# Kernel tuning notes

Measured on AMD Instinct MI355X. Metric: run time of the kernel, lower is better.

The kernel has to match this reference:

```python
import jax, jax.numpy as jnp
import numpy as np

B, T, HID = 2, 2048, 1536
H, HKV, D = 12, 2, 128
EPS = 1e-6
NEG = -1e9


def setup_inputs() -> dict:
    key = jax.random.key(0)
    ks = jax.random.split(key, 8)
    # rotary embeddings built from real angles (cos/sin of position*inv_freq)
    inv_freq = 1.0 / (10000.0 ** (jnp.arange(0, D, 2, dtype=jnp.float32) / D))  # [D/2]
    pos = jnp.arange(T, dtype=jnp.float32)
    ang = pos[:, None] * inv_freq[None, :]                       # [T, D/2]
    emb = jnp.concatenate([ang, ang], axis=-1)                   # [T, D]
    cos = jnp.broadcast_to(jnp.cos(emb)[None], (B, T, D))
    sin = jnp.broadcast_to(jnp.sin(emb)[None], (B, T, D))
    # additive causal mask [1,1,T,T]
    causal = jnp.tril(jnp.ones((T, T), dtype=bool))
    attention_mask = jnp.where(causal, 0.0, NEG).astype(jnp.float32)[None, None]
    s = 0.02
    return {
        "hidden_states": jax.random.normal(ks[0], (B, T, HID), jnp.float32),
        "cos": cos,
        "sin": sin,
        "attention_mask": attention_mask,
        "q_w": jax.random.normal(ks[1], (H * D, HID), jnp.float32) * s,
        "k_w": jax.random.normal(ks[2], (HKV * D, HID), jnp.float32) * s,
        "v_w": jax.random.normal(ks[3], (HKV * D, HID), jnp.float32) * s,
        "o_w": jax.random.normal(ks[4], (HID, H * D), jnp.float32) * s,
        "q_norm_w": jnp.ones((D,), jnp.float32),
        "k_norm_w": jnp.ones((D,), jnp.float32),
    }


def _rms_norm(x, w):
    # per-head RMSNorm over last dim (head_dim), computed in fp32
    xf = x.astype(jnp.float32)
    var = jnp.mean(xf * xf, axis=-1, keepdims=True)
    return (w * (xf * jax.lax.rsqrt(var + EPS))).astype(x.dtype)


def _rotate_half(x):
    x1, x2 = jnp.split(x, 2, axis=-1)
    return jnp.concatenate([-x2, x1], axis=-1)


def reference(hidden_states, cos, sin, attention_mask, q_w, k_w, v_w, o_w, q_norm_w, k_norm_w):
    b, t, _ = hidden_states.shape
    n_rep = H // HKV
    scale = D ** -0.5

    # projections -> [B, n_heads, T, D]
    q = (hidden_states @ q_w.T).reshape(b, t, H, D)
    k = (hidden_states @ k_w.T).reshape(b, t, HKV, D)
    v = (hidden_states @ v_w.T).reshape(b, t, HKV, D).transpose(0, 2, 1, 3)

    # per-head QK RMSNorm, then to [B, H, T, D]
    q = _rms_norm(q, q_norm_w).transpose(0, 2, 1, 3)
    k = _rms_norm(k, k_norm_w).transpose(0, 2, 1, 3)

    # RoPE (cos/sin broadcast over head axis)
    c = cos[:, None, :, :]
    s = sin[:, None, :, :]
    q = q * c + _rotate_half(q) * s
    k = k * c + _rotate_half(k) * s

    # GQA repeat_kv: [B, HKV, T, D] -> [B, H, T, D]
    k = jnp.repeat(k, n_rep, axis=1)
    v = jnp.repeat(v, n_rep, axis=1)

    attn = jnp.einsum('bhqd,bhkd->bhqk', q, k) * scale + attention_mask
    attn = jax.nn.softmax(attn.astype(jnp.float32), axis=-1).astype(q.dtype)
    out = jnp.einsum('bhqk,bhkd->bhqd', attn, v)
    out = out.transpose(0, 2, 1, 3).reshape(b, t, H * D)
    return out @ o_w.T
```

## Files before the change

### kernel.cpp

```cpp
#include <hip/hip_runtime.h>
#include <hip/hip_bf16.h>


#define B_   2
#define T_   2048
#define HID_ 1536
#define H_   12
#define HKV_ 2
#define D_   128
#define GQ_  (H_ / HKV_)
#define NQKV_ 2048
#define SCALE_ 0.08838834764831845f

typedef unsigned short u16;
typedef __attribute__((ext_vector_type(4))) float f32x4;
typedef __attribute__((ext_vector_type(8))) short bf16x8;
typedef __attribute__((ext_vector_type(4))) unsigned short u16x4;
typedef __attribute__((ext_vector_type(8))) unsigned short u16x8;

__device__ __forceinline__ u16 f2b(float f) {
  union { __hip_bfloat16 h; u16 u; } cv;
  cv.h = __float2bfloat16(f);
  return cv.u;
}
__device__ __forceinline__ float b2f(u16 u) {
  union { float f; unsigned i; } cv;
  cv.i = ((unsigned)u) << 16;
  return cv.f;
}

__device__ __forceinline__ void glds16(const u16* g, u16* l) {
  __builtin_amdgcn_global_load_lds((const __attribute__((address_space(1))) void*)g,
                                   (__attribute__((address_space(3))) void*)l, 16, 0, 0);
}

__global__ __launch_bounds__(256) void cvt_f32_bf16(const float* __restrict__ src,
                                                    u16* __restrict__ dst, int n4) {
  int i = blockIdx.x * 256 + threadIdx.x;
  const int stride = gridDim.x * 256;
  for (; i < n4; i += stride) {
    const float4 v = reinterpret_cast<const float4*>(src)[i];
    u16x4 o = {f2b(v.x), f2b(v.y), f2b(v.z), f2b(v.w)};
    reinterpret_cast<u16x4*>(dst)[i] = o;
  }
}

__device__ __forceinline__ void cstore(float* p, float v) { *p = v; }
__device__ __forceinline__ void cstore(u16* p, float v) { *p = f2b(v); }

template <typename CT>
__global__ __launch_bounds__(256) void gemm_bt(const u16* __restrict__ A,
                                               const u16* __restrict__ W,
                                               CT* __restrict__ C,
                                               int M, int N, int K) {
  __shared__ __align__(16) u16 As[128 * 32];
  __shared__ __align__(16) u16 Ws[128 * 32];
  const int tid  = threadIdx.x;
  const int lane = tid & 63;
  const int wid  = tid >> 6;
  const int wr = wid >> 1, wc = wid & 1;
  const int l15 = lane & 15, kg = lane >> 4;
  const int rowBase = blockIdx.y * 128;
  const int colBase = blockIdx.x * 128;

  const int srow = lane >> 2;
  const int scol = (lane & 3) << 3;
  const u16* Ab = A + (size_t)(rowBase + wid * 16 + srow) * K + scol;
  const u16* Wb = W + (size_t)(colBase + wid * 16 + srow) * K + scol;
  u16* AsW = &As[wid * 512];
  u16* WsW = &Ws[wid * 512];

  const f32x4 zero4 = {0.f, 0.f, 0.f, 0.f};
  f32x4 acc[4][4];
#pragma unroll
  for (int m = 0; m < 4; ++m)
#pragma unroll
    for (int n = 0; n < 4; ++n) acc[m][n] = zero4;

  for (int k0 = 0; k0 < K; k0 += 32) {
    __syncthreads();
    glds16(Ab + k0, AsW);
    glds16(Ab + (size_t)64 * K + k0, AsW + 2048);
    glds16(Wb + k0, WsW);
    glds16(Wb + (size_t)64 * K + k0, WsW + 2048);
    __syncthreads();
    bf16x8 a[4], b[4];
#pragma unroll
    for (int m = 0; m < 4; ++m)
      a[m] = *reinterpret_cast<const bf16x8*>(&As[(wr * 64 + m * 16 + l15) * 32 + kg * 8]);
#pragma unroll
    for (int n = 0; n < 4; ++n)
      b[n] = *reinterpret_cast<const bf16x8*>(&Ws[(wc * 64 + n * 16 + l15) * 32 + kg * 8]);
#pragma unroll
    for (int m = 0; m < 4; ++m)
#pragma unroll
      for (int n = 0; n < 4; ++n)
        acc[m][n] = __builtin_amdgcn_mfma_f32_16x16x32_bf16(a[m], b[n], acc[m][n], 0, 0, 0);
  }
#pragma unroll
  for (int m = 0; m < 4; ++m) {
    const int row0 = rowBase + wr * 64 + m * 16 + kg * 4;
#pragma unroll
    for (int n = 0; n < 4; ++n) {
      const int col = colBase + wc * 64 + n * 16 + l15;
#pragma unroll
      for (int r = 0; r < 4; ++r) cstore(&C[(size_t)(row0 + r) * N + col], acc[m][n][r]);
    }
  }
}

__global__ __launch_bounds__(256) void norm_rope_cvt(
    const u16* __restrict__ qkv, const float* __restrict__ cosb,
    const float* __restrict__ sinb, const float* __restrict__ q_nw,
    const float* __restrict__ k_nw, u16* __restrict__ q_b,
    u16* __restrict__ k_b, u16* __restrict__ vt_b) {
  const int gwave = (int)((blockIdx.x * 256 + threadIdx.x) >> 6);
  const int lane = threadIdx.x & 63;
  const int NQ = B_ * T_ * H_;
  const int NK = B_ * T_ * HKV_;
  if (gwave < NQ) {
    const int bt = gwave / H_, h = gwave - bt * H_;
    const u16* src = qkv + (size_t)bt * NQKV_ + h * D_;
    const float x1 = b2f(src[lane]), x2 = b2f(src[lane + 64]);
    float ss = x1 * x1 + x2 * x2;
#pragma unroll
    for (int m = 32; m >= 1; m >>= 1) ss += __shfl_xor(ss, m);
    const float rinv = rsqrtf(ss * (1.0f / D_) + 1e-6f);
    const float c1 = cosb[(size_t)bt * D_ + lane], c2 = cosb[(size_t)bt * D_ + lane + 64];
    const float s1 = sinb[(size_t)bt * D_ + lane], s2 = sinb[(size_t)bt * D_ + lane + 64];
    const float n1 = x1 * rinv * q_nw[lane], n2 = x2 * rinv * q_nw[lane + 64];
    const float o1 = (n1 * c1 - n2 * s1) * SCALE_;
    const float o2 = (n2 * c2 + n1 * s2) * SCALE_;
    const int b = bt >> 11, t = bt & (T_ - 1);
    u16* dst = q_b + ((size_t)(b * H_ + h) * T_ + t) * D_;
    dst[lane] = f2b(o1);
    dst[lane + 64] = f2b(o2);
  } else if (gwave < NQ + NK) {
    const int r = gwave - NQ;
    const int bt = r >> 1, hv = r & 1;
    const u16* src = qkv + (size_t)bt * NQKV_ + 1536 + hv * D_;
    const float x1 = b2f(src[lane]), x2 = b2f(src[lane + 64]);
    float ss = x1 * x1 + x2 * x2;
#pragma unroll
    for (int m = 32; m >= 1; m >>= 1) ss += __shfl_xor(ss, m);
    const float rinv = rsqrtf(ss * (1.0f / D_) + 1e-6f);
    const float c1 = cosb[(size_t)bt * D_ + lane], c2 = cosb[(size_t)bt * D_ + lane + 64];
    const float s1 = sinb[(size_t)bt * D_ + lane], s2 = sinb[(size_t)bt * D_ + lane + 64];
    const float n1 = x1 * rinv * k_nw[lane], n2 = x2 * rinv * k_nw[lane + 64];
    const float o1 = n1 * c1 - n2 * s1;
    const float o2 = n2 * c2 + n1 * s2;
    const int b = bt >> 11, t = bt & (T_ - 1);
    u16* dst = k_b + ((size_t)(b * HKV_ + hv) * T_ + t) * D_;
    dst[lane] = f2b(o1);
    dst[lane + 64] = f2b(o2);
  } else {
    const int r = gwave - NQ - NK;
    const int bt = r >> 1, hv = r & 1;
    const u16* src = qkv + (size_t)bt * NQKV_ + 1792 + hv * D_;
    const float x1 = b2f(src[lane]), x2 = b2f(src[lane + 64]);
    const int b = bt >> 11, t = bt & (T_ - 1);
    const int kk = t & 63;
    const int tp = (t & ~63) | (kk & 32) | (((kk >> 2) & 3) << 3) |
                   (((kk >> 4) & 1) << 2) | (kk & 3);
    u16* dst = vt_b + (size_t)(b * HKV_ + hv) * D_ * T_;
    dst[(size_t)lane * T_ + tp] = f2b(x1);
    dst[(size_t)(lane + 64) * T_ + tp] = f2b(x2);
  }
}

__global__ __launch_bounds__(256) void attn_kernel(const u16* __restrict__ q_b,
                                                   const u16* __restrict__ k_b,
                                                   const u16* __restrict__ vt_b,
                                                   u16* __restrict__ aout,
                                                   u16* __restrict__ po0,
                                                   float2* __restrict__ ml) {
  __shared__ __align__(16) u16 Ks[2][64 * 128];
  __shared__ __align__(16) u16 Vs[2][128 * 64];
  const int bh = blockIdx.x;
  const int y = blockIdx.y;
  const int qt = (y < 16) ? y : (y - 8);
  const int s = (y < 16) ? 0 : 1;
  const int kt0 = s * 16;
  const int ktend = (s == 0) ? min(2 * qt + 1, 15) : (2 * qt + 1);
  const bool splitq = (qt >= 8);
  const int b = bh / H_, h = bh - b * H_;
  const int kvh = h / GQ_;
  const int tid = threadIdx.x;
  const int w = tid >> 6, lane = tid & 63;
  const int l15 = lane & 15, kg = lane >> 4;
  const int qbase = qt * 128;

  const u16* Kb = k_b + (size_t)(b * HKV_ + kvh) * T_ * D_;
  const u16* Vb = vt_b + (size_t)(b * HKV_ + kvh) * D_ * T_;

  bf16x8 qf[2][4];
#pragma unroll
  for (int qb = 0; qb < 2; ++qb) {
    const u16* qrow =
        q_b + ((size_t)(b * H_ + h) * T_ + qbase + w * 32 + qb * 16 + l15) * D_;
#pragma unroll
    for (int s4 = 0; s4 < 4; ++s4)
      qf[qb][s4] = *reinterpret_cast<const bf16x8*>(qrow + s4 * 32 + kg * 8);
  }

  int kK[4], vK[4];
#pragma unroll
  for (int c = 0; c < 4; ++c) {
    const int ch = w * 4 + c;
    const int kr = ch * 4 + (lane >> 4);
    kK[c] = kr * D_ + (((lane & 15) << 3) ^ ((kr & 7) << 3));
    const int dr = ch * 8 + (lane >> 3);
    vK[c] = dr * T_ + (((lane & 7) << 3) ^ ((dr & 7) << 3));
  }

  const int xorv = (l15 & 7) << 3;

  const f32x4 zero4 = {0.f, 0.f, 0.f, 0.f};
  f32x4 o[2][8];
#pragma unroll
  for (int qb = 0; qb < 2; ++qb)
#pragma unroll
    for (int n = 0; n < 8; ++n) o[qb][n] = zero4;
  float m[2] = {0.f, 0.f};
  float lsum[2] = {0.f, 0.f};

  {
    const size_t kb = (size_t)kt0 * 64;
#pragma unroll
    for (int c = 0; c < 4; ++c) {
      glds16(Kb + kb * D_ + kK[c], &Ks[0][(w * 4 + c) * 512]);
      glds16(Vb + kb + vK[c], &Vs[0][(w * 4 + c) * 512]);
    }
  }
  __syncthreads();
  int cur = 0;

  for (int kt = kt0; kt <= ktend; ++kt) {
    if (kt < ktend) {
      const size_t kb = (size_t)(kt + 1) * 64;
#pragma unroll
      for (int c = 0; c < 4; ++c) {
        glds16(Kb + kb * D_ + kK[c], &Ks[cur ^ 1][(w * 4 + c) * 512]);
        glds16(Vb + kb + vK[c], &Vs[cur ^ 1][(w * 4 + c) * 512]);
      }
    }
    f32x4 sc[2][4];
#pragma unroll
    for (int qb = 0; qb < 2; ++qb)
#pragma unroll
      for (int n = 0; n < 4; ++n) sc[qb][n] = zero4;
#pragma unroll
    for (int n = 0; n < 4; ++n)
#pragma unroll
      for (int s4 = 0; s4 < 4; ++s4) {
        const int koff = (n * 16 + l15) * 128 + ((s4 * 32 + kg * 8) ^ xorv);
        bf16x8 kf = *reinterpret_cast<const bf16x8*>(&Ks[cur][koff]);
#pragma unroll
        for (int qb = 0; qb < 2; ++qb)
          sc[qb][n] = __builtin_amdgcn_mfma_f32_16x16x32_bf16(kf, qf[qb][s4],
                                                              sc[qb][n], 0, 0, 0);
      }
    if (kt >= 2 * qt) {
#pragma unroll
      for (int qb = 0; qb < 2; ++qb) {
        const int qg = w * 32 + qb * 16 + l15;
        const int kbb = (kt - 2 * qt) * 64;
#pragma unroll
        for (int n = 0; n < 4; ++n)
#pragma unroll
          for (int r = 0; r < 4; ++r)
            if (kbb + n * 16 + kg * 4 + r > qg) sc[qb][n][r] = -3e38f;
      }
    }
    float pm[2];
#pragma unroll
    for (int qb = 0; qb < 2; ++qb) {
      float v = sc[qb][0][0];
#pragma unroll
      for (int n = 0; n < 4; ++n)
#pragma unroll
        for (int r = 0; r < 4; ++r) v = fmaxf(v, sc[qb][n][r]);
      v = fmaxf(v, __shfl_xor(v, 16));
      v = fmaxf(v, __shfl_xor(v, 32));
      pm[qb] = v;
    }
    if (__any((pm[0] > m[0] + 8.f) | (pm[1] > m[1] + 8.f))) {
#pragma unroll
      for (int qb = 0; qb < 2; ++qb) {
        const float mn = fmaxf(m[qb], pm[qb]);
        const float al = __expf(m[qb] - mn);
        m[qb] = mn;
        lsum[qb] *= al;
        float alT[4];
#pragma unroll
        for (int r = 0; r < 4; ++r)
          alT[r] = __shfl(al, (lane & 48) | (kg * 4 + r));
#pragma unroll
        for (int n = 0; n < 8; ++n)
#pragma unroll
          for (int r = 0; r < 4; ++r) o[qb][n][r] *= alT[r];
      }
    }
#pragma unroll
    for (int qb = 0; qb < 2; ++qb) {
      float rs = 0.f;
#pragma unroll
      for (int n = 0; n < 4; ++n)
#pragma unroll
        for (int r = 0; r < 4; ++r) {
          const float p = __expf(sc[qb][n][r] - m[qb]);
          sc[qb][n][r] = p;
          rs += p;
        }
      rs += __shfl_xor(rs, 16);
      rs += __shfl_xor(rs, 32);
      lsum[qb] += rs;
    }
    bf16x8 pf[2][2];
#pragma unroll
    for (int qb = 0; qb < 2; ++qb)
#pragma unroll
      for (int ks = 0; ks < 2; ++ks)
#pragma unroll
        for (int r = 0; r < 4; ++r) {
          pf[qb][ks][r] = (short)f2b(sc[qb][2 * ks][r]);
          pf[qb][ks][r + 4] = (short)f2b(sc[qb][2 * ks + 1][r]);
        }
#pragma unroll
    for (int n = 0; n < 8; ++n)
#pragma unroll
      for (int ks = 0; ks < 2; ++ks) {
        const int voff = (n * 16 + l15) * 64 + ((ks * 32 + kg * 8) ^ xorv);
        bf16x8 vf = *reinterpret_cast<const bf16x8*>(&Vs[cur][voff]);
#pragma unroll
        for (int qb = 0; qb < 2; ++qb)
          o[qb][n] = __builtin_amdgcn_mfma_f32_16x16x32_bf16(pf[qb][ks], vf,
                                                             o[qb][n], 0, 0, 0);
      }
    if (kt < ktend) {
      __syncthreads();
      cur ^= 1;
    }
  }

  if (!splitq) {
    float invT[2][4];
#pragma unroll
    for (int qb = 0; qb < 2; ++qb) {
      const float inv = 1.0f / lsum[qb];
#pragma unroll
      for (int r = 0; r < 4; ++r)
        invT[qb][r] = __shfl(inv, (lane & 48) | (kg * 4 + r));
    }
#pragma unroll
    for (int qb = 0; qb < 2; ++qb) {
      const int t0 = qbase + w * 32 + qb * 16 + kg * 4;
#pragma unroll
      for (int n = 0; n < 8; ++n)
#pragma unroll
        for (int r = 0; r < 4; ++r)
          aout[(size_t)(b * T_ + t0 + r) * (H_ * D_) + h * D_ + n * 16 + l15] =
              f2b(o[qb][n][r] * invT[qb][r]);
    }
  } else {
    const int slot = bh * 8 + (qt - 8);
    if (kg == 0) {
#pragma unroll
      for (int qb = 0; qb < 2; ++qb) {
        float2 v;
        v.x = m[qb];
        v.y = lsum[qb];
        ml[(size_t)(slot * 2 + s) * 128 + w * 32 + qb * 16 + l15] = v;
      }
    }
    if (s == 1) {
#pragma unroll
      for (int qb = 0; qb < 2; ++qb) {
        const int t0 = qbase + w * 32 + qb * 16 + kg * 4;
#pragma unroll
        for (int n = 0; n < 8; ++n)
#pragma unroll
          for (int r = 0; r < 4; ++r)
            aout[(size_t)(b * T_ + t0 + r) * (H_ * D_) + h * D_ + n * 16 + l15] =
                f2b(o[qb][n][r]);
      }
    } else {
#pragma unroll
      for (int qb = 0; qb < 2; ++qb) {
        const int row0 = w * 32 + qb * 16 + kg * 4;
#pragma unroll
        for (int n = 0; n < 8; ++n)
#pragma unroll
          for (int r = 0; r < 4; ++r)
            po0[((size_t)slot * 128 + row0 + r) * 128 + n * 16 + l15] =
                f2b(o[qb][n][r]);
      }
    }
  }
}

__global__ __launch_bounds__(256) void combine_kernel(u16* __restrict__ aout,
                                                      const u16* __restrict__ po0,
                                                      const float2* __restrict__ ml) {
  const int bh = blockIdx.x;
  const int qt8 = blockIdx.y;
  const int slot = bh * 8 + qt8;
  const int b = bh / H_, h = bh - b * H_;
  const int t0 = (qt8 + 8) * 128;
  const int tid = threadIdx.x;
  const int row = tid >> 1;
  const int colc = (tid & 1) << 6;

  const float2 ml0 = ml[(size_t)(slot * 2 + 0) * 128 + row];
  const float2 ml1 = ml[(size_t)(slot * 2 + 1) * 128 + row];
  const float mm = fmaxf(ml0.x, ml1.x);
  const float c0 = __expf(ml0.x - mm), c1 = __expf(ml1.x - mm);
  const float inv = 1.0f / (ml0.y * c0 + ml1.y * c1);
  const float s0 = c0 * inv, s1 = c1 * inv;

  const u16* p0 = po0 + ((size_t)slot * 128 + row) * 128 + colc;
  u16* a = aout + (size_t)(b * T_ + t0 + row) * (H_ * D_) + h * D_ + colc;
#pragma unroll
  for (int j = 0; j < 8; ++j) {
    u16x8 v0 = *reinterpret_cast<const u16x8*>(p0 + j * 8);
    u16x8 v1 = *reinterpret_cast<const u16x8*>(a + j * 8);
    u16x8 outv;
#pragma unroll
    for (int e = 0; e < 8; ++e) outv[e] = f2b(b2f(v0[e]) * s0 + b2f(v1[e]) * s1);
    *reinterpret_cast<u16x8*>(a + j * 8) = outv;
  }
}

extern "C" void kernel_launch(void* const* d_in, const int* in_sizes, int n_in,
                              void* d_out, int out_size, void* d_ws, size_t ws_size,
                              hipStream_t stream) {
  const float* hidden = (const float*)d_in[0];
  const float* cosb   = (const float*)d_in[1];
  const float* sinb   = (const float*)d_in[2];
  const float* q_w  = (const float*)d_in[4];
  const float* k_w  = (const float*)d_in[5];
  const float* v_w  = (const float*)d_in[6];
  const float* o_w  = (const float*)d_in[7];
  const float* q_nw = (const float*)d_in[8];
  const float* k_nw = (const float*)d_in[9];
  float* out = (float*)d_out;

  char* ws = (char*)d_ws;
  const size_t MB = 1u << 20;
  u16*    hidden_b = (u16*)(ws);
  u16*    qkvw     = (u16*)(ws + 12 * MB);
  u16*    q_b      = (u16*)(ws);
  u16*    aout     = (u16*)(ws + 12 * MB);
  float2* ml       = (float2*)(ws + 24 * MB);
  u16*    k_b      = (u16*)(ws + 24 * MB + 512 * 1024);
  u16*    vt_b     = (u16*)(ws + 26 * MB + 512 * 1024);
  u16*    owb      = (u16*)(ws + 28 * MB + 512 * 1024);
  u16*    qkv_proj = (u16*)d_out;
  u16*    po0      = (u16*)d_out;

  const dim3 blk(256);
  const int M = B_ * T_;

  {
    const int nh = (B_ * T_ * HID_) / 4;
    const int nq = (H_ * D_ * HID_) / 4;
    const int nk = (HKV_ * D_ * HID_) / 4;
    cvt_f32_bf16<<<2048, blk, 0, stream>>>(hidden, hidden_b, nh);
    cvt_f32_bf16<<<2048, blk, 0, stream>>>(q_w, qkvw, nq);
    cvt_f32_bf16<<<384, blk, 0, stream>>>(k_w, qkvw + (size_t)1536 * HID_, nk);
    cvt_f32_bf16<<<384, blk, 0, stream>>>(v_w, qkvw + (size_t)1792 * HID_, nk);
    cvt_f32_bf16<<<2048, blk, 0, stream>>>(o_w, owb, nq);
  }

  gemm_bt<u16><<<dim3(NQKV_ / 128, M / 128), blk, 0, stream>>>(hidden_b, qkvw, qkv_proj,
                                                               M, NQKV_, HID_);

  norm_rope_cvt<<<16384, blk, 0, stream>>>(qkv_proj, cosb, sinb, q_nw, k_nw,
                                           q_b, k_b, vt_b);

  attn_kernel<<<dim3(B_ * H_, 24), blk, 0, stream>>>(q_b, k_b, vt_b, aout, po0, ml);
  combine_kernel<<<dim3(B_ * H_, 8), blk, 0, stream>>>(aout, po0, ml);

  gemm_bt<float><<<dim3(HID_ / 128, M / 128), blk, 0, stream>>>(aout, owb, out,
                                                                M, HID_, HID_);
}
```

Baseline: 206.5 us.

## Balance causal split-K work and single-buffer K/V tiles in LDS

Query tiles with index 8 and up are now split at their midpoint key tile, so both halves do equal work; before, the split was at a fixed tile 16, which left the halves uneven. Heavy and light work items are interleaved across blockIdx.y to even out scheduling. The K/V double buffer in shared memory becomes a single buffer with a barrier before and after each tile load. This halves LDS use per block and may allow more resident blocks, but it gives up the overlap of the next tile's load with the current tile's compute.

```diff
diff --git a/kernel.cpp b/kernel.cpp
--- a/kernel.cpp
+++ b/kernel.cpp
@@ -174,15 +174,20 @@
                                                    u16* __restrict__ aout,
                                                    u16* __restrict__ po0,
                                                    float2* __restrict__ ml) {
-  __shared__ __align__(16) u16 Ks[2][64 * 128];
-  __shared__ __align__(16) u16 Vs[2][128 * 64];
+  __shared__ __align__(16) u16 Ks[64 * 128];
+  __shared__ __align__(16) u16 Vs[128 * 64];
   const int bh = blockIdx.x;
   const int y = blockIdx.y;
-  const int qt = (y < 16) ? y : (y - 8);
-  const int s = (y < 16) ? 0 : 1;
-  const int kt0 = s * 16;
-  const int ktend = (s == 0) ? min(2 * qt + 1, 15) : (2 * qt + 1);
-  const bool splitq = (qt >= 8);
+  const int item = (y & 1) ? (23 - (y >> 1)) : (y >> 1);
+  int qt, s, kt0, ktend;
+  bool splitq;
+  if (item < 8) {
+    qt = item; s = 0; kt0 = 0; ktend = 2 * qt + 1; splitq = false;
+  } else if (item < 16) {
+    qt = item; s = 0; kt0 = 0; ktend = qt; splitq = true;
+  } else {
+    qt = item - 8; s = 1; kt0 = qt + 1; ktend = 2 * qt + 1; splitq = true;
+  }
   const int b = bh / H_, h = bh - b * H_;
   const int kvh = h / GQ_;
   const int tid = threadIdx.x;
@@ -224,26 +229,17 @@
   float m[2] = {0.f, 0.f};
   float lsum[2] = {0.f, 0.f};
 
-  {
-    const size_t kb = (size_t)kt0 * 64;
-#pragma unroll
-    for (int c = 0; c < 4; ++c) {
-      glds16(Kb + kb * D_ + kK[c], &Ks[0][(w * 4 + c) * 512]);
-      glds16(Vb + kb + vK[c], &Vs[0][(w * 4 + c) * 512]);
-    }
-  }
-  __syncthreads();
-  int cur = 0;
-
   for (int kt = kt0; kt <= ktend; ++kt) {
-    if (kt < ktend) {
-      const size_t kb = (size_t)(kt + 1) * 64;
+    __syncthreads();
+    {
+      const size_t kb = (size_t)kt * 64;
 #pragma unroll
       for (int c = 0; c < 4; ++c) {
-        glds16(Kb + kb * D_ + kK[c], &Ks[cur ^ 1][(w * 4 + c) * 512]);
-        glds16(Vb + kb + vK[c], &Vs[cur ^ 1][(w * 4 + c) * 512]);
-      }
-    }
+        glds16(Kb + kb * D_ + kK[c], &Ks[(w * 4 + c) * 512]);
+        glds16(Vb + kb + vK[c], &Vs[(w * 4 + c) * 512]);
+      }
+    }
+    __syncthreads();
     f32x4 sc[2][4];
 #pragma unroll
     for (int qb = 0; qb < 2; ++qb)
@@ -254,7 +250,7 @@
 #pragma unroll
       for (int s4 = 0; s4 < 4; ++s4) {
         const int koff = (n * 16 + l15) * 128 + ((s4 * 32 + kg * 8) ^ xorv);
-        bf16x8 kf = *reinterpret_cast<const bf16x8*>(&Ks[cur][koff]);
+        bf16x8 kf = *reinterpret_cast<const bf16x8*>(&Ks[koff]);
 #pragma unroll
         for (int qb = 0; qb < 2; ++qb)
           sc[qb][n] = __builtin_amdgcn_mfma_f32_16x16x32_bf16(kf, qf[qb][s4],
@@ -331,16 +327,12 @@
 #pragma unroll
       for (int ks = 0; ks < 2; ++ks) {
         const int voff = (n * 16 + l15) * 64 + ((ks * 32 + kg * 8) ^ xorv);
-        bf16x8 vf = *reinterpret_cast<const bf16x8*>(&Vs[cur][voff]);
+        bf16x8 vf = *reinterpret_cast<const bf16x8*>(&Vs[voff]);
 #pragma unroll
         for (int qb = 0; qb < 2; ++qb)
           o[qb][n] = __builtin_amdgcn_mfma_f32_16x16x32_bf16(pf[qb][ks], vf,
                                                              o[qb][n], 0, 0, 0);
       }
-    if (kt < ktend) {
-      __syncthreads();
-      cur ^= 1;
-    }
   }
 
   if (!splitq) {
```

New measurement: 197.4 us. 1.05x faster.
